# Performance work log

Hardware: AMD Instinct MI355X
Metric: run time of the kernel (lower is better)

The kernel has to match this reference:

```python
import jax, jax.numpy as jnp
import numpy as np

B, S, D, DQKV = 4, 2048, 1024, 1024

def setup_inputs() -> dict:
    key = jax.random.key(0)
    kx, kq, kk, kv = jax.random.split(key, 4)
    scale = 1.0 / np.sqrt(D)
    return {
        "x": jax.random.normal(kx, (B, S, D), dtype=jnp.float32),
        "wq": jax.random.normal(kq, (D, DQKV), dtype=jnp.float32) * scale,
        "wk": jax.random.normal(kk, (D, DQKV), dtype=jnp.float32) * scale,
        "wv": jax.random.normal(kv, (D, DQKV), dtype=jnp.float32) * scale,
    }

def reference(x, wq, wk, wv):
    # QKV projections: [B,S,D] @ [D,Dqkv] -> [B,S,Dqkv]
    q = jnp.einsum('bsd,de->bse', x, wq)
    k = jnp.einsum('bsd,de->bse', x, wk)
    v = jnp.einsum('bsd,de->bse', x, wv)
    # scores: [B,S,S], scaled by sqrt(dim_qkv)
    scores = jnp.einsum('bik,bjk->bij', q, k) / jnp.sqrt(jnp.asarray(DQKV, dtype=x.dtype))
    attn = jax.nn.softmax(scores, axis=-1)
    # output: [B,S,Dqkv]
    return jnp.einsum('bij,bjd->bid', attn, v)
```

## Files before the change

kernel.cpp:

```cpp
#include <hip/hip_runtime.h>
#include <cstdint>
#include <cstddef>

typedef __bf16 bf16;
typedef __bf16 bf16x4 __attribute__((ext_vector_type(4)));
typedef __bf16 bf16x8 __attribute__((ext_vector_type(8)));
typedef float  f32x4  __attribute__((ext_vector_type(4)));

#define BATCH 4
#define SEQ   2048
#define DIM   1024

__device__ __forceinline__ bf16 to_bf16(float f) {
    unsigned u = __builtin_bit_cast(unsigned, f);
    u += 0x7fffu + ((u >> 16) & 1u);
    unsigned short h = (unsigned short)(u >> 16);
    return __builtin_bit_cast(bf16, h);
}

__device__ __forceinline__ void load16_lds(const bf16* g, bf16* l) {
    __builtin_amdgcn_global_load_lds(
        (__attribute__((address_space(1))) void*)(g),
        (__attribute__((address_space(3))) void*)(l),
        16, 0, 0);
}

template<int BM>
__device__ __forceinline__ void gemm_core64(
    const bf16* __restrict__ Abase, const bf16* __restrict__ Bbase,
    int K, int lda, int ldb, bf16* As, bf16* Bs, f32x4 acc[BM / 32][4])
{
    constexpr int MI = BM / 32;
    const int tid  = threadIdx.x;
    const int lane = tid & 63;
    const int wave = tid >> 6;
    const int wm   = (wave >> 1) * (BM / 2);
    const int wn   = (wave & 1) * 64;
    const int r16  = lane & 15;
    const int g    = lane >> 4;
    const int srow0 = wave * 8 + (lane >> 3);
    const int scoff = (((lane & 7) ^ ((lane >> 3) & 7)) * 8);
    const int ldsW  = wave * 512;

    for (int k0 = 0; k0 < K; k0 += 64) {
        __syncthreads();
#pragma unroll
        for (int j = 0; j < BM / 32; ++j)
            load16_lds(Abase + (size_t)(j * 32 + srow0) * lda + k0 + scoff,
                       As + j * 2048 + ldsW);
#pragma unroll
        for (int j = 0; j < 4; ++j)
            load16_lds(Bbase + (size_t)(j * 32 + srow0) * ldb + k0 + scoff,
                       Bs + j * 2048 + ldsW);
        __syncthreads();

#pragma unroll
        for (int h = 0; h < 2; ++h) {
            bf16x8 af[MI], bfr[4];
            const int p = (h * 4 + g) ^ (r16 & 7);
#pragma unroll
            for (int i = 0; i < MI; ++i)
                af[i]  = *(const bf16x8*)(As + (wm + i * 16 + r16) * 64 + p * 8);
#pragma unroll
            for (int i = 0; i < 4; ++i)
                bfr[i] = *(const bf16x8*)(Bs + (wn + i * 16 + r16) * 64 + p * 8);
#pragma unroll
            for (int mi = 0; mi < MI; ++mi)
#pragma unroll
                for (int ni = 0; ni < 4; ++ni)
                    acc[mi][ni] = __builtin_amdgcn_mfma_f32_16x16x32_bf16(
                        af[mi], bfr[ni], acc[mi][ni], 0, 0, 0);
        }
    }
}

__global__ __launch_bounds__(256, 4) void proj_gemm(
    const bf16* __restrict__ xb, const bf16* __restrict__ Wt,
    bf16* __restrict__ QK, bf16* __restrict__ Vt)
{
    __shared__ bf16 As[8192];
    __shared__ bf16 Bs[8192];
    f32x4 acc[4][4] = {};

    const int r = blockIdx.x;
    const bf16 *Ab, *Bb;
    bf16* Cb;
    int bx, byl;
    if (r < 1024) {
        const int c = r & 7, j = r >> 3;
        bx  = j & 15;
        byl = c + 8 * (j >> 4);
        Ab = xb + (size_t)byl * 128 * DIM;
        Bb = Wt + (size_t)bx * 128 * DIM;
        Cb = QK + (size_t)byl * 128 * 2048;
    } else {
        const int u = r - 1024;
        const int c = u & 7, j = u >> 3;
        bx = j & 15;
        const int p = c + 8 * (j >> 4);
        byl = p & 7;
        const int bz = p >> 3;
        Ab = Wt + (size_t)2 * DIM * DIM + (size_t)byl * 128 * DIM;
        Bb = xb + (size_t)bz * SEQ * DIM + (size_t)bx * 128 * DIM;
        Cb = Vt + (size_t)bz * DIM * SEQ + (size_t)byl * 128 * 2048;
    }
    gemm_core64<128>(Ab, Bb, DIM, DIM, DIM, As, Bs, acc);

    const int lane = threadIdx.x & 63;
    const int wave = threadIdx.x >> 6;
    const int wm = (wave >> 1) * 64, wn = (wave & 1) * 64;
    const int rowO = wm + ((lane >> 4) * 4);
    const int colO = bx * 128 + wn + (lane & 15);
#pragma unroll
    for (int mi = 0; mi < 4; ++mi)
#pragma unroll
        for (int ni = 0; ni < 4; ++ni)
#pragma unroll
            for (int rr = 0; rr < 4; ++rr)
                Cb[(size_t)(rowO + mi * 16 + rr) * 2048 + colO + ni * 16] =
                    to_bf16(acc[mi][ni][rr]);
}

__global__ __launch_bounds__(256, 4) void gemm_scores(
    const bf16* __restrict__ A, const bf16* __restrict__ Bm, bf16* __restrict__ C,
    float* __restrict__ lsum)
{
    __shared__ bf16 As[8192];
    __shared__ bf16 Bs[8192];
    f32x4 acc[4][4] = {};

    const int d = blockIdx.x + 16 * (blockIdx.y + 16 * blockIdx.z);
    const int c = d & 7, j = d >> 3;
    const int bx = j & 15;
    const int p = c + 8 * (j >> 4);
    const int by = p & 15, bz = p >> 4;

    const int lda = 2 * DIM;
    const bf16* Ab = A  + (size_t)bz * SEQ * lda + (size_t)by * 128 * lda;
    const bf16* Bb = Bm + (size_t)bz * SEQ * lda + (size_t)bx * 128 * lda;
    bf16* Cb = C + (size_t)bz * SEQ * SEQ;
    gemm_core64<128>(Ab, Bb, DIM, lda, lda, As, Bs, acc);

    const int lane = threadIdx.x & 63;
    const int wave = threadIdx.x >> 6;
    const int wm = (wave >> 1) * 64, wn = (wave & 1) * 64;
    const int rowBase = by * 128 + wm + ((lane >> 4) * 4);
    const int colBase = bx * 128 + wn + (lane & 15);

#pragma unroll
    for (int mi = 0; mi < 4; ++mi)
#pragma unroll
        for (int ni = 0; ni < 4; ++ni)
#pragma unroll
            for (int rr = 0; rr < 4; ++rr) {
                const float e = __expf(acc[mi][ni][rr] * 0.03125f);
                acc[mi][ni][rr] = e;
                Cb[(size_t)(rowBase + mi * 16 + rr) * SEQ + colBase + ni * 16] =
                    to_bf16(e);
            }

    float* ls = lsum + (size_t)bz * SEQ;
#pragma unroll
    for (int mi = 0; mi < 4; ++mi)
#pragma unroll
        for (int rr = 0; rr < 4; ++rr) {
            float s = acc[mi][0][rr] + acc[mi][1][rr] + acc[mi][2][rr] + acc[mi][3][rr];
            s += __shfl_xor(s, 1);
            s += __shfl_xor(s, 2);
            s += __shfl_xor(s, 4);
            s += __shfl_xor(s, 8);
            if ((lane & 15) == 0)
                atomicAdd(ls + rowBase + mi * 16 + rr, s);
        }
}

__global__ __launch_bounds__(256, 4) void gemm_pv(
    const bf16* __restrict__ A, const bf16* __restrict__ Bm, float* __restrict__ C,
    const float* __restrict__ lsum)
{
    __shared__ bf16 As[4096];
    __shared__ bf16 Bs[8192];
    f32x4 acc[2][4] = {};

    const int d = blockIdx.x + 8 * (blockIdx.y + 32 * blockIdx.z);
    const int c = d & 7, j = d >> 3;
    const int bx = j & 7;
    const int p = c + 8 * (j >> 3);
    const int by = p & 31, bz = p >> 5;

    const bf16* Ab = A  + (size_t)bz * SEQ * SEQ + (size_t)by * 64 * SEQ;
    const bf16* Bb = Bm + (size_t)bz * DIM * SEQ + (size_t)bx * 128 * SEQ;
    float* Cb = C + (size_t)bz * SEQ * DIM;
    gemm_core64<64>(Ab, Bb, SEQ, SEQ, SEQ, As, Bs, acc);

    const int lane = threadIdx.x & 63;
    const int wave = threadIdx.x >> 6;
    const int wm = (wave >> 1) * 32, wn = (wave & 1) * 64;
    const int rowBase = by * 64 + wm + ((lane >> 4) * 4);
    const int colBase = bx * 128 + wn + (lane & 15);
    const float* ls = lsum + (size_t)bz * SEQ;
#pragma unroll
    for (int mi = 0; mi < 2; ++mi)
#pragma unroll
        for (int rr = 0; rr < 4; ++rr) {
            const float inv = __builtin_amdgcn_rcpf(ls[rowBase + mi * 16 + rr]);
#pragma unroll
            for (int ni = 0; ni < 4; ++ni)
                Cb[(size_t)(rowBase + mi * 16 + rr) * DIM + colBase + ni * 16] =
                    acc[mi][ni][rr] * inv;
        }
}

__global__ __launch_bounds__(256) void prep(
    const float* __restrict__ x,  const float* __restrict__ wq,
    const float* __restrict__ wk, const float* __restrict__ wv,
    bf16* __restrict__ xb, bf16* __restrict__ Wt, float* __restrict__ lsum)
{
    __shared__ float tile[32][33];
    const int b = blockIdx.x;
    const int tid = threadIdx.x;
    if (b < 8192) {
        const size_t i = ((size_t)b * 256 + tid) * 4;
        const float4 v = *(const float4*)(x + i);
        bf16x4 o = { to_bf16(v.x), to_bf16(v.y), to_bf16(v.z), to_bf16(v.w) };
        *(bf16x4*)(xb + i) = o;
    } else if (b < 8192 + 3072) {
        const int t   = b - 8192;
        const int sel = t >> 10;
        const int n0  = (t & 31) * 32;
        const int k0  = ((t >> 5) & 31) * 32;
        const float* w = (sel == 0) ? wq : (sel == 1) ? wk : wv;
        const int tx = tid & 31, ty = tid >> 5;
#pragma unroll
        for (int j = 0; j < 32; j += 8)
            tile[ty + j][tx] = w[(size_t)(k0 + ty + j) * 1024 + n0 + tx];
        __syncthreads();
        bf16* dst = Wt + (size_t)sel * 1024 * 1024;
#pragma unroll
        for (int j = 0; j < 32; j += 8)
            dst[(size_t)(n0 + ty + j) * 1024 + k0 + tx] = to_bf16(tile[tx][ty + j]);
    } else {
#pragma unroll
        for (int i = 0; i < 32; ++i)
            lsum[i * 256 + tid] = 0.0f;
    }
}

extern "C" void kernel_launch(void* const* d_in, const int* in_sizes, int n_in,
                              void* d_out, int out_size, void* d_ws, size_t ws_size,
                              hipStream_t stream)
{
    const float* x  = (const float*)d_in[0];
    const float* wq = (const float*)d_in[1];
    const float* wk = (const float*)d_in[2];
    const float* wv = (const float*)d_in[3];
    float* out = (float*)d_out;
    char* ws = (char*)d_ws;

    bf16*  xb   = (bf16*)(ws);
    bf16*  Wt   = (bf16*)(ws + (16u << 20));
    bf16*  QK   = (bf16*)(ws + (22u << 20));
    bf16*  Vt   = (bf16*)(ws + (54u << 20));
    bf16*  P    = (bf16*)(ws + (70u << 20));
    float* lsum = (float*)(ws + (102u << 20));

    prep<<<dim3(8192 + 3072 + 1), dim3(256), 0, stream>>>(
        x, wq, wk, wv, xb, Wt, lsum);

    proj_gemm<<<dim3(1536), dim3(256), 0, stream>>>(xb, Wt, QK, Vt);

    gemm_scores<<<dim3(16, 16, 4), dim3(256), 0, stream>>>(QK, QK + DIM, P, lsum);

    gemm_pv<<<dim3(8, 32, 4), dim3(256), 0, stream>>>(P, Vt, out, lsum);
}
```

Before: 237.4 us.

## Split-K PV GEMM with 128x128 tiles and atomic accumulation

The PV GEMM moves from 64x128 tiles over full K=2048 to 128x128 tiles with K split into two halves. Partial results are combined with float atomicAdd into an output that is zeroed by a memset first. This aims to improve per-tile data reuse while keeping the block count the same, at the cost of an extra memset and atomic traffic. Launch bounds on the projection and scores kernels are raised from 4 to 5 blocks per CU, which may force register spills.

```diff
diff --git a/kernel.cpp b/kernel.cpp
--- a/kernel.cpp
+++ b/kernel.cpp
@@ -25,16 +25,14 @@
         16, 0, 0);
 }
 
-template<int BM>
 __device__ __forceinline__ void gemm_core64(
     const bf16* __restrict__ Abase, const bf16* __restrict__ Bbase,
-    int K, int lda, int ldb, bf16* As, bf16* Bs, f32x4 acc[BM / 32][4])
-{
-    constexpr int MI = BM / 32;
+    int K, int lda, int ldb, bf16* As, bf16* Bs, f32x4 acc[4][4])
+{
     const int tid  = threadIdx.x;
     const int lane = tid & 63;
     const int wave = tid >> 6;
-    const int wm   = (wave >> 1) * (BM / 2);
+    const int wm   = (wave >> 1) * 64;
     const int wn   = (wave & 1) * 64;
     const int r16  = lane & 15;
     const int g    = lane >> 4;
@@ -45,27 +43,25 @@
     for (int k0 = 0; k0 < K; k0 += 64) {
         __syncthreads();
 #pragma unroll
-        for (int j = 0; j < BM / 32; ++j)
+        for (int j = 0; j < 4; ++j) {
             load16_lds(Abase + (size_t)(j * 32 + srow0) * lda + k0 + scoff,
                        As + j * 2048 + ldsW);
-#pragma unroll
-        for (int j = 0; j < 4; ++j)
             load16_lds(Bbase + (size_t)(j * 32 + srow0) * ldb + k0 + scoff,
                        Bs + j * 2048 + ldsW);
+        }
         __syncthreads();
 
 #pragma unroll
         for (int h = 0; h < 2; ++h) {
-            bf16x8 af[MI], bfr[4];
+            bf16x8 af[4], bfr[4];
             const int p = (h * 4 + g) ^ (r16 & 7);
 #pragma unroll
-            for (int i = 0; i < MI; ++i)
+            for (int i = 0; i < 4; ++i) {
                 af[i]  = *(const bf16x8*)(As + (wm + i * 16 + r16) * 64 + p * 8);
-#pragma unroll
-            for (int i = 0; i < 4; ++i)
                 bfr[i] = *(const bf16x8*)(Bs + (wn + i * 16 + r16) * 64 + p * 8);
-#pragma unroll
-            for (int mi = 0; mi < MI; ++mi)
+            }
+#pragma unroll
+            for (int mi = 0; mi < 4; ++mi)
 #pragma unroll
                 for (int ni = 0; ni < 4; ++ni)
                     acc[mi][ni] = __builtin_amdgcn_mfma_f32_16x16x32_bf16(
@@ -74,7 +70,7 @@
     }
 }
 
-__global__ __launch_bounds__(256, 4) void proj_gemm(
+__global__ __launch_bounds__(256, 5) void proj_gemm(
     const bf16* __restrict__ xb, const bf16* __restrict__ Wt,
     bf16* __restrict__ QK, bf16* __restrict__ Vt)
 {
@@ -104,7 +100,7 @@
         Bb = xb + (size_t)bz * SEQ * DIM + (size_t)bx * 128 * DIM;
         Cb = Vt + (size_t)bz * DIM * SEQ + (size_t)byl * 128 * 2048;
     }
-    gemm_core64<128>(Ab, Bb, DIM, DIM, DIM, As, Bs, acc);
+    gemm_core64(Ab, Bb, DIM, DIM, DIM, As, Bs, acc);
 
     const int lane = threadIdx.x & 63;
     const int wave = threadIdx.x >> 6;
@@ -121,7 +117,7 @@
                     to_bf16(acc[mi][ni][rr]);
 }
 
-__global__ __launch_bounds__(256, 4) void gemm_scores(
+__global__ __launch_bounds__(256, 5) void gemm_scores(
     const bf16* __restrict__ A, const bf16* __restrict__ Bm, bf16* __restrict__ C,
     float* __restrict__ lsum)
 {
@@ -139,7 +135,7 @@
     const bf16* Ab = A  + (size_t)bz * SEQ * lda + (size_t)by * 128 * lda;
     const bf16* Bb = Bm + (size_t)bz * SEQ * lda + (size_t)bx * 128 * lda;
     bf16* Cb = C + (size_t)bz * SEQ * SEQ;
-    gemm_core64<128>(Ab, Bb, DIM, lda, lda, As, Bs, acc);
+    gemm_core64(Ab, Bb, DIM, lda, lda, As, Bs, acc);
 
     const int lane = threadIdx.x & 63;
     const int wave = threadIdx.x >> 6;
@@ -178,36 +174,38 @@
     const bf16* __restrict__ A, const bf16* __restrict__ Bm, float* __restrict__ C,
     const float* __restrict__ lsum)
 {
-    __shared__ bf16 As[4096];
+    __shared__ bf16 As[8192];
     __shared__ bf16 Bs[8192];
-    f32x4 acc[2][4] = {};
-
-    const int d = blockIdx.x + 8 * (blockIdx.y + 32 * blockIdx.z);
+    f32x4 acc[4][4] = {};
+
+    const int d = blockIdx.x + 8 * (blockIdx.y + 16 * blockIdx.z);
     const int c = d & 7, j = d >> 3;
     const int bx = j & 7;
     const int p = c + 8 * (j >> 3);
-    const int by = p & 31, bz = p >> 5;
-
-    const bf16* Ab = A  + (size_t)bz * SEQ * SEQ + (size_t)by * 64 * SEQ;
-    const bf16* Bb = Bm + (size_t)bz * DIM * SEQ + (size_t)bx * 128 * SEQ;
+    const int by = p & 15;
+    const int z  = p >> 4;
+    const int bz = z >> 1, half = z & 1;
+
+    const bf16* Ab = A  + (size_t)bz * SEQ * SEQ + (size_t)by * 128 * SEQ + half * 1024;
+    const bf16* Bb = Bm + (size_t)bz * DIM * SEQ + (size_t)bx * 128 * SEQ + half * 1024;
     float* Cb = C + (size_t)bz * SEQ * DIM;
-    gemm_core64<64>(Ab, Bb, SEQ, SEQ, SEQ, As, Bs, acc);
+    gemm_core64(Ab, Bb, 1024, SEQ, SEQ, As, Bs, acc);
 
     const int lane = threadIdx.x & 63;
     const int wave = threadIdx.x >> 6;
-    const int wm = (wave >> 1) * 32, wn = (wave & 1) * 64;
-    const int rowBase = by * 64 + wm + ((lane >> 4) * 4);
+    const int wm = (wave >> 1) * 64, wn = (wave & 1) * 64;
+    const int rowBase = by * 128 + wm + ((lane >> 4) * 4);
     const int colBase = bx * 128 + wn + (lane & 15);
     const float* ls = lsum + (size_t)bz * SEQ;
 #pragma unroll
-    for (int mi = 0; mi < 2; ++mi)
+    for (int mi = 0; mi < 4; ++mi)
 #pragma unroll
         for (int rr = 0; rr < 4; ++rr) {
             const float inv = __builtin_amdgcn_rcpf(ls[rowBase + mi * 16 + rr]);
 #pragma unroll
             for (int ni = 0; ni < 4; ++ni)
-                Cb[(size_t)(rowBase + mi * 16 + rr) * DIM + colBase + ni * 16] =
-                    acc[mi][ni][rr] * inv;
+                atomicAdd(&Cb[(size_t)(rowBase + mi * 16 + rr) * DIM + colBase + ni * 16],
+                          acc[mi][ni][rr] * inv);
         }
 }
 
@@ -264,6 +262,8 @@
     bf16*  P    = (bf16*)(ws + (70u << 20));
     float* lsum = (float*)(ws + (102u << 20));
 
+    hipMemsetAsync(out, 0, (size_t)BATCH * SEQ * DIM * sizeof(float), stream);
+
     prep<<<dim3(8192 + 3072 + 1), dim3(256), 0, stream>>>(
         x, wq, wk, wv, xb, Wt, lsum);
 
@@ -271,5 +271,5 @@
 
     gemm_scores<<<dim3(16, 16, 4), dim3(256), 0, stream>>>(QK, QK + DIM, P, lsum);
 
-    gemm_pv<<<dim3(8, 32, 4), dim3(256), 0, stream>>>(P, Vt, out, lsum);
-}
+    gemm_pv<<<dim3(8, 16, 8), dim3(256), 0, stream>>>(P, Vt, out, lsum);
+}
```

New measurement: 444.5 us. 87.2% more time.
